# Kernel optimization log

Measured on AMD Instinct MI355X. Metric: run time of the kernel, lower is better.

The kernel has to match this reference:

```python
import jax, jax.numpy as jnp
import numpy as np

C_LIGHT = 1.0
G_NEWTON = 1.0
COUPLING = 8.0 * np.pi * G_NEWTON / C_LIGHT ** 4  # 8*pi*G/c^4


def _green_kernel():
    # 7x7 Green's-function kernel for Poisson eq: -1/(2*pi*r), center 0
    size, center = 7, 3
    k = np.zeros((1, 1, size, size), np.float32)
    for i in range(size):
        for j in range(size):
            r = np.sqrt((i - center) ** 2 + (j - center) ** 2)
            if r > 0:
                k[0, 0, i, j] = -1.0 / (2.0 * np.pi * r)
    return jnp.asarray(k)


def _gauss_kernel(C):
    # 3x3 separable Gaussian, sigma=1, depthwise (C,1,3,3)
    coords = np.arange(3, dtype=np.float32) - 1.0
    g = np.exp(-coords ** 2 / 2.0)
    g = g / g.sum()
    k = (g[None, :] * g[:, None]).astype(np.float32)
    return jnp.tile(jnp.asarray(k)[None, None], (C, 1, 1, 1))


def _conv(x, k, pad, groups=1):
    return jax.lax.conv_general_dilated(
        x, k, window_strides=(1, 1), padding=[(pad, pad), (pad, pad)],
        dimension_numbers=('NCHW', 'OIHW', 'NCHW'), feature_group_count=groups)


def setup_inputs() -> dict:
    key = jax.random.key(0)
    ks = jax.random.split(key, 20)
    B, H, W = 8, 256, 256
    p = lambda k, shape: (jax.random.normal(k, shape, jnp.float32) * 0.1)
    return {
        'mass': jax.random.uniform(ks[0], (B, H, W, 1), jnp.float32),
        'velocity': jax.random.normal(ks[1], (B, 3), jnp.float32),
        'metric_init': jax.random.normal(ks[2], (B, H, W, 10), jnp.float32),
        # energy net: Linear(4,64) -> GELU -> Linear(64,1) -> Softplus
        'e_w1': p(ks[3], (4, 64)), 'e_b1': jnp.zeros((64,), jnp.float32),
        'e_w2': p(ks[4], (64, 1)), 'e_b2': jnp.zeros((1,), jnp.float32),
        # momentum net: Linear(4,64) -> GELU -> Linear(64,3)
        'm_w1': p(ks[5], (4, 64)), 'm_b1': jnp.zeros((64,), jnp.float32),
        'm_w2': p(ks[6], (64, 3)), 'm_b2': jnp.zeros((3,), jnp.float32),
        # stress net: Linear(4,128) -> GELU -> Linear(128,6)
        's_w1': p(ks[7], (4, 128)), 's_b1': jnp.zeros((128,), jnp.float32),
        's_w2': p(ks[8], (128, 6)), 's_b2': jnp.zeros((6,), jnp.float32),
        'solver_params': jnp.asarray([0.5, 0.3, 0.2], jnp.float32),
    }


def reference(mass, velocity, metric_init,
              e_w1, e_b1, e_w2, e_b2,
              m_w1, m_b1, m_w2, m_b2,
              s_w1, s_b1, s_w2, s_b2,
              solver_params):
    B, H, W, _ = mass.shape
    gelu = lambda x: jax.nn.gelu(x, approximate=False)  # torch exact GELU

    # --- EnergyMomentumTensor: per-pixel MLPs ---
    vel = jnp.broadcast_to(velocity[:, None, None, :], (B, H, W, 3))
    inp = jnp.concatenate([mass, vel], axis=-1).reshape(B * H * W, 4)
    energy = jax.nn.softplus(gelu(inp @ e_w1 + e_b1) @ e_w2 + e_b2)   # [N,1]
    momentum = gelu(inp @ m_w1 + m_b1) @ m_w2 + m_b2                  # [N,3]
    stress = gelu(inp @ s_w1 + s_b1) @ s_w2 + s_b2                    # [N,6]
    T = jnp.concatenate([energy, momentum, stress], axis=-1).reshape(B, H, W, 10)

    # --- EinsteinFieldSolver (linearized) ---
    weights = jax.nn.softmax(solver_params)
    metric = metric_init + weights[0] * (-COUPLING * T)

    mass_n = mass / (mass.max() + 1e-8)
    pot = _conv(mass_n.transpose(0, 3, 1, 2), _green_kernel(), pad=3)[:, 0]  # [B,H,W]
    corr = jnp.zeros((B, H, W, 10), metric.dtype)
    corr = corr.at[..., 4].set(2.0 * G_NEWTON * pot).at[..., 7].set(2.0 * G_NEWTON * pot)
    metric = metric + weights[1] * corr

    # ensure metric validity (signature constraints on diagonal components)
    metric = metric.at[..., 0].set(jnp.minimum(metric[..., 0], -0.1))
    metric = metric.at[..., 4].set(jnp.maximum(metric[..., 4], 0.1))
    metric = metric.at[..., 7].set(jnp.maximum(metric[..., 7], 0.1))
    metric = metric.at[..., 9].set(jnp.maximum(metric[..., 9], 0.1))

    # conditional Gaussian smoothing (weights[2] > 0.1)
    smooth = _conv(metric.transpose(0, 3, 1, 2), _gauss_kernel(10), pad=1,
                   groups=10).transpose(0, 2, 3, 1)
    metric = jnp.where(weights[2] > 0.1, smooth, metric)
    return metric
```

## Files before the change

kernel.cpp:

```cpp
#include <hip/hip_runtime.h>
#include <hip/hip_bf16.h>
#include <math.h>

#define GH 256
#define GW 256
#define NC 10
#define NKNOT 257

__device__ __forceinline__ float gelu_exact(float x) {
    return 0.5f * x * (1.0f + erff(x * 0.70710678118654752f));
}
__device__ __forceinline__ float softplus_f(float x) {
    if (x > 20.f) return x;
    return log1pf(expf(x));
}

__global__ __launch_bounds__(256) void k_pre(
        const float* __restrict__ mass,
        const float* __restrict__ vel,
        const float* __restrict__ e_w1, const float* __restrict__ e_b1,
        const float* __restrict__ e_w2, const float* __restrict__ e_b2,
        const float* __restrict__ m_w1, const float* __restrict__ m_b1,
        const float* __restrict__ m_w2, const float* __restrict__ m_b2,
        const float* __restrict__ s_w1, const float* __restrict__ s_b1,
        const float* __restrict__ s_w2, const float* __restrict__ s_b2,
        float* __restrict__ ws) {
    const int tid = threadIdx.x;
    if (blockIdx.x >= 514) {
        const int pb = blockIdx.x - 514;
        const float4* mass4 = (const float4*)mass;
        int base = pb * 512 + tid;
        float4 a = mass4[base];
        float4 c = mass4[base + 256];
        float v = fmaxf(fmaxf(fmaxf(a.x, a.y), fmaxf(a.z, a.w)),
                        fmaxf(fmaxf(c.x, c.y), fmaxf(c.z, c.w)));
        #pragma unroll
        for (int off = 32; off > 0; off >>= 1)
            v = fmaxf(v, __shfl_xor(v, off, 64));
        __shared__ float sred[4];
        if ((tid & 63) == 0) sred[tid >> 6] = v;
        __syncthreads();
        if (tid == 0)
            ws[pb] = fmaxf(fmaxf(sred[0], sred[1]), fmaxf(sred[2], sred[3]));
        return;
    }
    const int wave = blockIdx.x * 4 + (tid >> 6);
    const int lane = tid & 63;
    const int b = wave / NKNOT, knot = wave % NKNOT;
    const float m = (float)knot * (1.0f / 256.0f);
    const float vx = vel[b * 3 + 0], vy = vel[b * 3 + 1], vz = vel[b * 3 + 2];

    float acc[10];
    {
        float pre = m * e_w1[lane] + vx * e_w1[64 + lane] + vy * e_w1[128 + lane]
                  + vz * e_w1[192 + lane] + e_b1[lane];
        acc[0] = gelu_exact(pre) * e_w2[lane];
    }
    {
        float pre = m * m_w1[lane] + vx * m_w1[64 + lane] + vy * m_w1[128 + lane]
                  + vz * m_w1[192 + lane] + m_b1[lane];
        float h = gelu_exact(pre);
        acc[1] = h * m_w2[lane * 3 + 0];
        acc[2] = h * m_w2[lane * 3 + 1];
        acc[3] = h * m_w2[lane * 3 + 2];
    }
    {
        float pre0 = m * s_w1[lane] + vx * s_w1[128 + lane] + vy * s_w1[256 + lane]
                   + vz * s_w1[384 + lane] + s_b1[lane];
        float pre1 = m * s_w1[64 + lane] + vx * s_w1[192 + lane] + vy * s_w1[320 + lane]
                   + vz * s_w1[448 + lane] + s_b1[64 + lane];
        float h0 = gelu_exact(pre0), h1 = gelu_exact(pre1);
        #pragma unroll
        for (int k = 0; k < 6; k++)
            acc[4 + k] = h0 * s_w2[lane * 6 + k] + h1 * s_w2[(lane + 64) * 6 + k];
    }
    #pragma unroll
    for (int c = 0; c < 10; c++) {
        float v = acc[c];
        #pragma unroll
        for (int off = 32; off > 0; off >>= 1)
            v += __shfl_xor(v, off, 64);
        acc[c] = v;
    }
    if (lane == 0) {
        float* lut = ws + 1024 + (size_t)(b * NKNOT + knot) * NC;
        lut[0] = softplus_f(acc[0] + e_b2[0]);
        lut[1] = acc[1] + m_b2[0];
        lut[2] = acc[2] + m_b2[1];
        lut[3] = acc[3] + m_b2[2];
        #pragma unroll
        for (int k = 0; k < 6; k++) lut[4 + k] = acc[4 + k] + s_b2[k];
    }
}

__global__ __launch_bounds__(256, 2) void k_main(const float* __restrict__ mass,
                                                 const float* __restrict__ minit,
                                                 const float* __restrict__ solver,
                                                 const float* __restrict__ ws,
                                                 float* __restrict__ out) {
    const int b = blockIdx.z;
    const int tid = threadIdx.x;
    const int tile_x = blockIdx.x * 32, tile_y = blockIdx.y * 32;

    __shared__ float  s_mass[40][44];
    __shared__ float2 s_met2[5][34][34];
    __shared__ float2 s_lut2[NKNOT * 6];
    __shared__ float  s_wmax[4];

    {
        float v = ws[tid];
        #pragma unroll
        for (int off = 32; off > 0; off >>= 1)
            v = fmaxf(v, __shfl_xor(v, off, 64));
        if ((tid & 63) == 0) s_wmax[tid >> 6] = v;
    }
    {
        const float2* lutg2 = (const float2*)(ws + 1024 + (size_t)b * NKNOT * NC);
        for (int i = tid; i < NKNOT * 5; i += 256) {
            int k = i / 5, c = i % 5;
            s_lut2[k * 6 + c] = lutg2[i];
        }
    }
    {
        const float* massb = mass + (size_t)b * GH * GW;
        for (int i = tid; i < 40 * 22; i += 256) {
            int my = i / 22, jx = i % 22;
            int gy = tile_y - 4 + my, gx = tile_x - 4 + 2 * jx;
            float2 v = make_float2(0.f, 0.f);
            if ((unsigned)gy < GH && (unsigned)gx < GW)
                v = *(const float2*)(massb + gy * GW + gx);
            *(float2*)&s_mass[my][2 * jx] = v;
        }
    }
    float p0 = solver[0], p1 = solver[1], p2 = solver[2];
    float pm = fmaxf(p0, fmaxf(p1, p2));
    float e0 = expf(p0 - pm), e1 = expf(p1 - pm), e2 = expf(p2 - pm);
    float inv = 1.f / (e0 + e1 + e2);
    float w0 = e0 * inv, w1 = e1 * inv, w2 = e2 * inv;

    __syncthreads();

    const float gmax = fmaxf(fmaxf(s_wmax[0], s_wmax[1]), fmaxf(s_wmax[2], s_wmax[3]));
    const float k0 = -25.132741228718345f * w0;
    const float potscale = 2.f * w1 / (gmax + 1e-8f);

    constexpr float GWt[4][4] = {
        {0.f,            -0.15915494f, -0.07957747f, -0.05305165f},
        {-0.15915494f,   -0.11253954f, -0.07117625f, -0.05033165f},
        {-0.07957747f,   -0.07117625f, -0.05626977f, -0.04414183f},
        {-0.05305165f,   -0.05033165f, -0.04414183f, -0.03751318f}};

    for (int item = tid; item < 17 * 17; item += 256) {
        const int py = item / 17, px = item % 17;
        const int ry0 = 2 * py, rx0 = 2 * px;
        float potTL = 0.f, potTR = 0.f, potBL = 0.f, potBR = 0.f;
        #pragma unroll
        for (int k = 0; k < 8; k++) {
            const float2* mr = (const float2*)&s_mass[ry0 + k][rx0];
            float v[10];
            #pragma unroll
            for (int h = 0; h < 5; h++) {
                float2 t = mr[h];
                v[2 * h] = t.x; v[2 * h + 1] = t.y;
            }
            #pragma unroll
            for (int j = 0; j < 10; j++) {
                const int dyt = k - 3, dyb = k - 4;
                const int dxl = j - 3, dxr = j - 4;
                const int at = dyt < 0 ? -dyt : dyt, ab = dyb < 0 ? -dyb : dyb;
                const int al = dxl < 0 ? -dxl : dxl, ar = dxr < 0 ? -dxr : dxr;
                if (k <= 6 && j <= 6 && !(k == 3 && j == 3)) potTL += GWt[at][al] * v[j];
                if (k <= 6 && j >= 1 && j <= 7 && !(k == 3 && j == 4)) potTR += GWt[at][ar] * v[j];
                if (k >= 1 && j <= 6 && !(k == 4 && j == 3)) potBL += GWt[ab][al] * v[j];
                if (k >= 1 && j >= 1 && j <= 7 && !(k == 4 && j == 4)) potBR += GWt[ab][ar] * v[j];
            }
        }
        const float pots[4] = {potTL, potTR, potBL, potBR};
        #pragma unroll
        for (int p = 0; p < 4; p++) {
            const int ry = ry0 + (p >> 1), rx = rx0 + (p & 1);
            const int gy = tile_y + ry - 1, gx = tile_x + rx - 1;
            if ((unsigned)gy >= GH || (unsigned)gx >= GW) {
                #pragma unroll
                for (int cp = 0; cp < 5; cp++)
                    s_met2[cp][ry][rx] = make_float2(0.f, 0.f);
                continue;
            }
            const float m = s_mass[ry + 3][rx + 3];
            const float potterm = potscale * pots[p];
            float x = m * 256.f;
            int i0 = (int)x;
            i0 = i0 < 255 ? i0 : 255;
            const float f = x - (float)i0;
            const float4* L0 = (const float4*)&s_lut2[i0 * 6];
            const float4* L1 = (const float4*)&s_lut2[(i0 + 1) * 6];
            float4 a01 = L0[0], a23 = L0[1];
            float4 b01 = L1[0], b23 = L1[1];
            float2 a4 = s_lut2[i0 * 6 + 4], b4 = s_lut2[(i0 + 1) * 6 + 4];
            const float2* mi2 = (const float2*)(minit + ((size_t)(b * GH + gy) * GW + gx) * NC);
            float2 mi0 = mi2[0], mi1 = mi2[1], mi2v = mi2[2], mi3 = mi2[3], mi4 = mi2[4];
            float2 r;
            r.x = fmaf(k0, fmaf(f, b01.x - a01.x, a01.x), mi0.x);
            r.y = fmaf(k0, fmaf(f, b01.y - a01.y, a01.y), mi0.y);
            r.x = fminf(r.x, -0.1f);
            s_met2[0][ry][rx] = r;
            r.x = fmaf(k0, fmaf(f, b01.z - a01.z, a01.z), mi1.x);
            r.y = fmaf(k0, fmaf(f, b01.w - a01.w, a01.w), mi1.y);
            s_met2[1][ry][rx] = r;
            r.x = fmaf(k0, fmaf(f, b23.x - a23.x, a23.x), mi2v.x) + potterm;
            r.y = fmaf(k0, fmaf(f, b23.y - a23.y, a23.y), mi2v.y);
            r.x = fmaxf(r.x, 0.1f);
            s_met2[2][ry][rx] = r;
            r.x = fmaf(k0, fmaf(f, b23.z - a23.z, a23.z), mi3.x);
            r.y = fmaf(k0, fmaf(f, b23.w - a23.w, a23.w), mi3.y) + potterm;
            r.y = fmaxf(r.y, 0.1f);
            s_met2[3][ry][rx] = r;
            r.x = fmaf(k0, fmaf(f, b4.x - a4.x, a4.x), mi4.x);
            r.y = fmaf(k0, fmaf(f, b4.y - a4.y, a4.y), mi4.y);
            r.y = fmaxf(r.y, 0.1f);
            s_met2[4][ry][rx] = r;
        }
    }
    __syncthreads();

    const int py = tid >> 4, px = tid & 15;
    const int oy0 = 2 * py, ox0 = 2 * px;
    const float g0 = 0.274068619f, g1 = 0.451862761f;
    const bool do_smooth = (w2 > 0.1f);
    float2 res[4][5];
    #pragma unroll
    for (int cp = 0; cp < 5; cp++) {
        float2 c0[4], c1[4], c2[4], c3[4];
        #pragma unroll
        for (int rr = 0; rr < 4; rr++) {
            const float4* row = (const float4*)&s_met2[cp][oy0 + rr][ox0];
            float4 a = row[0], bq = row[1];
            c0[rr] = make_float2(a.x, a.y);
            c1[rr] = make_float2(a.z, a.w);
            c2[rr] = make_float2(bq.x, bq.y);
            c3[rr] = make_float2(bq.z, bq.w);
        }
        if (do_smooth) {
            float2 HL[4], HR[4];
            #pragma unroll
            for (int rr = 0; rr < 4; rr++) {
                HL[rr].x = fmaf(g0, c0[rr].x + c2[rr].x, g1 * c1[rr].x);
                HL[rr].y = fmaf(g0, c0[rr].y + c2[rr].y, g1 * c1[rr].y);
                HR[rr].x = fmaf(g0, c1[rr].x + c3[rr].x, g1 * c2[rr].x);
                HR[rr].y = fmaf(g0, c1[rr].y + c3[rr].y, g1 * c2[rr].y);
            }
            res[0][cp].x = fmaf(g0, HL[0].x + HL[2].x, g1 * HL[1].x);
            res[0][cp].y = fmaf(g0, HL[0].y + HL[2].y, g1 * HL[1].y);
            res[1][cp].x = fmaf(g0, HR[0].x + HR[2].x, g1 * HR[1].x);
            res[1][cp].y = fmaf(g0, HR[0].y + HR[2].y, g1 * HR[1].y);
            res[2][cp].x = fmaf(g0, HL[1].x + HL[3].x, g1 * HL[2].x);
            res[2][cp].y = fmaf(g0, HL[1].y + HL[3].y, g1 * HL[2].y);
            res[3][cp].x = fmaf(g0, HR[1].x + HR[3].x, g1 * HR[2].x);
            res[3][cp].y = fmaf(g0, HR[1].y + HR[3].y, g1 * HR[2].y);
        } else {
            res[0][cp] = c1[1];
            res[1][cp] = c2[1];
            res[2][cp] = c1[2];
            res[3][cp] = c2[2];
        }
    }
    #pragma unroll
    for (int p = 0; p < 4; p++) {
        const int oy = oy0 + (p >> 1), ox = ox0 + (p & 1);
        float2* dst = (float2*)(out + ((size_t)(b * GH + tile_y + oy) * GW + tile_x + ox) * NC);
        #pragma unroll
        for (int cp = 0; cp < 5; cp++) dst[cp] = res[p][cp];
    }
}

extern "C" void kernel_launch(void* const* d_in, const int* in_sizes, int n_in,
                              void* d_out, int out_size, void* d_ws, size_t ws_size,
                              hipStream_t stream) {
    const float* mass   = (const float*)d_in[0];
    const float* vel    = (const float*)d_in[1];
    const float* minit  = (const float*)d_in[2];
    const float* e_w1   = (const float*)d_in[3];
    const float* e_b1   = (const float*)d_in[4];
    const float* e_w2   = (const float*)d_in[5];
    const float* e_b2   = (const float*)d_in[6];
    const float* m_w1   = (const float*)d_in[7];
    const float* m_b1   = (const float*)d_in[8];
    const float* m_w2   = (const float*)d_in[9];
    const float* m_b2   = (const float*)d_in[10];
    const float* s_w1   = (const float*)d_in[11];
    const float* s_b1   = (const float*)d_in[12];
    const float* s_w2   = (const float*)d_in[13];
    const float* s_b2   = (const float*)d_in[14];
    const float* solver = (const float*)d_in[15];
    float* ws  = (float*)d_ws;
    float* out = (float*)d_out;

    k_pre<<<770, 256, 0, stream>>>(mass, vel, e_w1, e_b1, e_w2, e_b2,
                                   m_w1, m_b1, m_w2, m_b2,
                                   s_w1, s_b1, s_w2, s_b2, ws);
    dim3 grid(8, 8, 8);
    k_main<<<grid, 256, 0, stream>>>(mass, minit, solver, ws, out);
}
```

Baseline: 30.09 us.

## Shrink main tile to 16x16, stage metric_init and output through LDS

The main kernel tile shrinks from 32x32 to 16x16, which quadruples the grid to 2048 blocks and raises the launch-bounds occupancy hint to 4. metric_init is prefetched cooperatively into shared memory, and results go through a shared buffer before coalesced float4 stores, replacing per-thread strided float2 global accesses. The aim is better occupancy and coalesced memory traffic. The cost is more halo overhead (18x18 rows staged per 16x16 outputs), an extra barrier, and potential-convolution work that now runs on only 81 of 256 threads.

```diff
diff --git a/kernel.cpp b/kernel.cpp
--- a/kernel.cpp
+++ b/kernel.cpp
@@ -93,18 +93,19 @@
     }
 }
 
-__global__ __launch_bounds__(256, 2) void k_main(const float* __restrict__ mass,
+__global__ __launch_bounds__(256, 4) void k_main(const float* __restrict__ mass,
                                                  const float* __restrict__ minit,
                                                  const float* __restrict__ solver,
                                                  const float* __restrict__ ws,
                                                  float* __restrict__ out) {
     const int b = blockIdx.z;
     const int tid = threadIdx.x;
-    const int tile_x = blockIdx.x * 32, tile_y = blockIdx.y * 32;
-
-    __shared__ float  s_mass[40][44];
-    __shared__ float2 s_met2[5][34][34];
-    __shared__ float2 s_lut2[NKNOT * 6];
+    const int tile_x = blockIdx.x * 16, tile_y = blockIdx.y * 16;
+
+    __shared__ float  s_mass[24][24];
+    __shared__ float2 s_lut2[NKNOT * 5];
+    __shared__ float2 s_met2[5][18][18];
+    __shared__ __align__(16) float2 s_minout[18 * 90];
     __shared__ float  s_wmax[4];
 
     {
@@ -116,15 +117,24 @@
     }
     {
         const float2* lutg2 = (const float2*)(ws + 1024 + (size_t)b * NKNOT * NC);
-        for (int i = tid; i < NKNOT * 5; i += 256) {
-            int k = i / 5, c = i % 5;
-            s_lut2[k * 6 + c] = lutg2[i];
+        for (int i = tid; i < NKNOT * 5; i += 256) s_lut2[i] = lutg2[i];
+    }
+    {
+        const float* mb = minit + (size_t)b * GH * GW * NC;
+        for (int i = tid; i < 18 * 90; i += 256) {
+            int r = i / 90, c2 = i % 90;
+            int px = c2 / 5;
+            int gy = tile_y - 1 + r, gx = tile_x - 1 + px;
+            float2 v = make_float2(0.f, 0.f);
+            if ((unsigned)gy < GH && (unsigned)gx < GW)
+                v = *(const float2*)(mb + ((size_t)gy * GW + gx) * NC + (c2 % 5) * 2);
+            s_minout[i] = v;
         }
     }
     {
         const float* massb = mass + (size_t)b * GH * GW;
-        for (int i = tid; i < 40 * 22; i += 256) {
-            int my = i / 22, jx = i % 22;
+        for (int i = tid; i < 24 * 12; i += 256) {
+            int my = i / 12, jx = i % 12;
             int gy = tile_y - 4 + my, gx = tile_x - 4 + 2 * jx;
             float2 v = make_float2(0.f, 0.f);
             if ((unsigned)gy < GH && (unsigned)gx < GW)
@@ -145,34 +155,34 @@
     const float potscale = 2.f * w1 / (gmax + 1e-8f);
 
     constexpr float GWt[4][4] = {
-        {0.f,            -0.15915494f, -0.07957747f, -0.05305165f},
-        {-0.15915494f,   -0.11253954f, -0.07117625f, -0.05033165f},
-        {-0.07957747f,   -0.07117625f, -0.05626977f, -0.04414183f},
-        {-0.05305165f,   -0.05033165f, -0.04414183f, -0.03751318f}};
-
-    for (int item = tid; item < 17 * 17; item += 256) {
-        const int py = item / 17, px = item % 17;
+        {0.f,          -0.15915494f, -0.07957747f, -0.05305165f},
+        {-0.15915494f, -0.11253954f, -0.07117625f, -0.05033165f},
+        {-0.07957747f, -0.07117625f, -0.05626977f, -0.04414183f},
+        {-0.05305165f, -0.05033165f, -0.04414183f, -0.03751318f}};
+
+    for (int item = tid; item < 9 * 9; item += 256) {
+        const int py = item / 9, px = item % 9;
         const int ry0 = 2 * py, rx0 = 2 * px;
         float potTL = 0.f, potTR = 0.f, potBL = 0.f, potBR = 0.f;
         #pragma unroll
         for (int k = 0; k < 8; k++) {
             const float2* mr = (const float2*)&s_mass[ry0 + k][rx0];
-            float v[10];
+            float v[8];
             #pragma unroll
-            for (int h = 0; h < 5; h++) {
+            for (int h = 0; h < 4; h++) {
                 float2 t = mr[h];
                 v[2 * h] = t.x; v[2 * h + 1] = t.y;
             }
             #pragma unroll
-            for (int j = 0; j < 10; j++) {
+            for (int j = 0; j < 8; j++) {
                 const int dyt = k - 3, dyb = k - 4;
                 const int dxl = j - 3, dxr = j - 4;
                 const int at = dyt < 0 ? -dyt : dyt, ab = dyb < 0 ? -dyb : dyb;
                 const int al = dxl < 0 ? -dxl : dxl, ar = dxr < 0 ? -dxr : dxr;
                 if (k <= 6 && j <= 6 && !(k == 3 && j == 3)) potTL += GWt[at][al] * v[j];
-                if (k <= 6 && j >= 1 && j <= 7 && !(k == 3 && j == 4)) potTR += GWt[at][ar] * v[j];
+                if (k <= 6 && j >= 1 && !(k == 3 && j == 4)) potTR += GWt[at][ar] * v[j];
                 if (k >= 1 && j <= 6 && !(k == 4 && j == 3)) potBL += GWt[ab][al] * v[j];
-                if (k >= 1 && j >= 1 && j <= 7 && !(k == 4 && j == 4)) potBR += GWt[ab][ar] * v[j];
+                if (k >= 1 && j >= 1 && !(k == 4 && j == 4)) potBR += GWt[ab][ar] * v[j];
             }
         }
         const float pots[4] = {potTL, potTR, potBL, potBR};
@@ -192,84 +202,62 @@
             int i0 = (int)x;
             i0 = i0 < 255 ? i0 : 255;
             const float f = x - (float)i0;
-            const float4* L0 = (const float4*)&s_lut2[i0 * 6];
-            const float4* L1 = (const float4*)&s_lut2[(i0 + 1) * 6];
-            float4 a01 = L0[0], a23 = L0[1];
-            float4 b01 = L1[0], b23 = L1[1];
-            float2 a4 = s_lut2[i0 * 6 + 4], b4 = s_lut2[(i0 + 1) * 6 + 4];
-            const float2* mi2 = (const float2*)(minit + ((size_t)(b * GH + gy) * GW + gx) * NC);
-            float2 mi0 = mi2[0], mi1 = mi2[1], mi2v = mi2[2], mi3 = mi2[3], mi4 = mi2[4];
-            float2 r;
-            r.x = fmaf(k0, fmaf(f, b01.x - a01.x, a01.x), mi0.x);
-            r.y = fmaf(k0, fmaf(f, b01.y - a01.y, a01.y), mi0.y);
-            r.x = fminf(r.x, -0.1f);
-            s_met2[0][ry][rx] = r;
-            r.x = fmaf(k0, fmaf(f, b01.z - a01.z, a01.z), mi1.x);
-            r.y = fmaf(k0, fmaf(f, b01.w - a01.w, a01.w), mi1.y);
-            s_met2[1][ry][rx] = r;
-            r.x = fmaf(k0, fmaf(f, b23.x - a23.x, a23.x), mi2v.x) + potterm;
-            r.y = fmaf(k0, fmaf(f, b23.y - a23.y, a23.y), mi2v.y);
-            r.x = fmaxf(r.x, 0.1f);
-            s_met2[2][ry][rx] = r;
-            r.x = fmaf(k0, fmaf(f, b23.z - a23.z, a23.z), mi3.x);
-            r.y = fmaf(k0, fmaf(f, b23.w - a23.w, a23.w), mi3.y) + potterm;
-            r.y = fmaxf(r.y, 0.1f);
-            s_met2[3][ry][rx] = r;
-            r.x = fmaf(k0, fmaf(f, b4.x - a4.x, a4.x), mi4.x);
-            r.y = fmaf(k0, fmaf(f, b4.y - a4.y, a4.y), mi4.y);
-            r.y = fmaxf(r.y, 0.1f);
-            s_met2[4][ry][rx] = r;
+            const float2* L0 = &s_lut2[i0 * 5];
+            const float2* L1 = &s_lut2[i0 * 5 + 5];
+            const float2* mi2 = &s_minout[(ry * 18 + rx) * 5];
+            #pragma unroll
+            for (int cp = 0; cp < 5; cp++) {
+                float2 t0 = L0[cp], t1 = L1[cp], mi = mi2[cp];
+                float2 r;
+                r.x = fmaf(k0, fmaf(f, t1.x - t0.x, t0.x), mi.x);
+                r.y = fmaf(k0, fmaf(f, t1.y - t0.y, t0.y), mi.y);
+                if (cp == 2) r.x += potterm;
+                if (cp == 3) r.y += potterm;
+                if (cp == 0) r.x = fminf(r.x, -0.1f);
+                if (cp == 2) r.x = fmaxf(r.x, 0.1f);
+                if (cp == 3) r.y = fmaxf(r.y, 0.1f);
+                if (cp == 4) r.y = fmaxf(r.y, 0.1f);
+                s_met2[cp][ry][rx] = r;
+            }
         }
     }
     __syncthreads();
 
-    const int py = tid >> 4, px = tid & 15;
-    const int oy0 = 2 * py, ox0 = 2 * px;
-    const float g0 = 0.274068619f, g1 = 0.451862761f;
-    const bool do_smooth = (w2 > 0.1f);
-    float2 res[4][5];
-    #pragma unroll
-    for (int cp = 0; cp < 5; cp++) {
-        float2 c0[4], c1[4], c2[4], c3[4];
-        #pragma unroll
-        for (int rr = 0; rr < 4; rr++) {
-            const float4* row = (const float4*)&s_met2[cp][oy0 + rr][ox0];
-            float4 a = row[0], bq = row[1];
-            c0[rr] = make_float2(a.x, a.y);
-            c1[rr] = make_float2(a.z, a.w);
-            c2[rr] = make_float2(bq.x, bq.y);
-            c3[rr] = make_float2(bq.z, bq.w);
-        }
-        if (do_smooth) {
-            float2 HL[4], HR[4];
-            #pragma unroll
-            for (int rr = 0; rr < 4; rr++) {
-                HL[rr].x = fmaf(g0, c0[rr].x + c2[rr].x, g1 * c1[rr].x);
-                HL[rr].y = fmaf(g0, c0[rr].y + c2[rr].y, g1 * c1[rr].y);
-                HR[rr].x = fmaf(g0, c1[rr].x + c3[rr].x, g1 * c2[rr].x);
-                HR[rr].y = fmaf(g0, c1[rr].y + c3[rr].y, g1 * c2[rr].y);
-            }
-            res[0][cp].x = fmaf(g0, HL[0].x + HL[2].x, g1 * HL[1].x);
-            res[0][cp].y = fmaf(g0, HL[0].y + HL[2].y, g1 * HL[1].y);
-            res[1][cp].x = fmaf(g0, HR[0].x + HR[2].x, g1 * HR[1].x);
-            res[1][cp].y = fmaf(g0, HR[0].y + HR[2].y, g1 * HR[1].y);
-            res[2][cp].x = fmaf(g0, HL[1].x + HL[3].x, g1 * HL[2].x);
-            res[2][cp].y = fmaf(g0, HL[1].y + HL[3].y, g1 * HL[2].y);
-            res[3][cp].x = fmaf(g0, HR[1].x + HR[3].x, g1 * HR[2].x);
-            res[3][cp].y = fmaf(g0, HR[1].y + HR[3].y, g1 * HR[2].y);
-        } else {
-            res[0][cp] = c1[1];
-            res[1][cp] = c2[1];
-            res[2][cp] = c1[2];
-            res[3][cp] = c2[2];
-        }
-    }
-    #pragma unroll
-    for (int p = 0; p < 4; p++) {
-        const int oy = oy0 + (p >> 1), ox = ox0 + (p & 1);
-        float2* dst = (float2*)(out + ((size_t)(b * GH + tile_y + oy) * GW + tile_x + ox) * NC);
-        #pragma unroll
-        for (int cp = 0; cp < 5; cp++) dst[cp] = res[p][cp];
+    {
+        const int oy = tid >> 4, ox = tid & 15;
+        float2* s_out2 = s_minout;
+        const float g0 = 0.274068619f, g1 = 0.451862761f;
+        const bool do_smooth = (w2 > 0.1f);
+        #pragma unroll
+        for (int cp = 0; cp < 5; cp++) {
+            float2 v;
+            if (do_smooth) {
+                float2 a0 = s_met2[cp][oy][ox],     a1 = s_met2[cp][oy][ox + 1],     a2 = s_met2[cp][oy][ox + 2];
+                float2 b0 = s_met2[cp][oy + 1][ox], b1 = s_met2[cp][oy + 1][ox + 1], b2 = s_met2[cp][oy + 1][ox + 2];
+                float2 c0 = s_met2[cp][oy + 2][ox], c1 = s_met2[cp][oy + 2][ox + 1], c2 = s_met2[cp][oy + 2][ox + 2];
+                float r0x = fmaf(g0, a0.x + a2.x, g1 * a1.x);
+                float r0y = fmaf(g0, a0.y + a2.y, g1 * a1.y);
+                float r1x = fmaf(g0, b0.x + b2.x, g1 * b1.x);
+                float r1y = fmaf(g0, b0.y + b2.y, g1 * b1.y);
+                float r2x = fmaf(g0, c0.x + c2.x, g1 * c1.x);
+                float r2y = fmaf(g0, c0.y + c2.y, g1 * c1.y);
+                v.x = fmaf(g0, r0x + r2x, g1 * r1x);
+                v.y = fmaf(g0, r0y + r2y, g1 * r1y);
+            } else {
+                v = s_met2[cp][oy + 1][ox + 1];
+            }
+            s_out2[(oy * 16 + ox) * 5 + cp] = v;
+        }
+    }
+    __syncthreads();
+
+    {
+        const float4* s_out4 = (const float4*)s_minout;
+        float* ob = out + ((size_t)(b * GH + tile_y) * GW + tile_x) * NC;
+        for (int i = tid; i < 16 * 40; i += 256) {
+            int r = i / 40, c4 = i % 40;
+            *(float4*)(ob + (size_t)r * GW * NC + c4 * 4) = s_out4[r * 40 + c4];
+        }
     }
 }
 
@@ -298,6 +286,6 @@
     k_pre<<<770, 256, 0, stream>>>(mass, vel, e_w1, e_b1, e_w2, e_b2,
                                    m_w1, m_b1, m_w2, m_b2,
                                    s_w1, s_b1, s_w2, s_b2, ws);
-    dim3 grid(8, 8, 8);
+    dim3 grid(16, 16, 8);
     k_main<<<grid, 256, 0, stream>>>(mass, minit, solver, ws, out);
 }
```

Result: slower. 35.27 us (+17.2%).
